# Optimization experiments

Hardware: AMD Instinct MI355X
Metric: run time of the kernel (lower is better)

## Reference

```python
import jax, jax.numpy as jnp
import numpy as np

B, TOK, D, H, L = 64, 20, 512, 8, 4
S = 512          # tokens per half
HD = D // H
ODIM = 32        # encoder_output_dim


def _ln(x, g, b):
    m = x.mean(-1, keepdims=True)
    v = ((x - m) ** 2).mean(-1, keepdims=True)
    return (x - m) / jnp.sqrt(v + 1e-5) * g + b


def _alibi_slopes(h):
    # mirrors FlashAttentionBlock.build_alibi_slopes (base=2.0)
    base = 2.0
    return jnp.asarray([1.0 / base ** (i // (h // base)) for i in range(h)], dtype=jnp.float32)


def setup_inputs() -> dict:
    key = jax.random.key(0)
    ks = jax.random.split(key, 16)
    r = lambda i, shape, s=0.02: jax.random.normal(ks[i], shape, jnp.float32) * s
    return {
        'x': jax.random.normal(ks[0], (B, 2 * S * TOK), jnp.float32),
        'in_W': r(1, (TOK, D)), 'in_b': jnp.zeros((D,)),
        'qkv_W': r(2, (L, D, 3 * D)), 'qkv_b': jnp.zeros((L, 3 * D)),
        'ln1_g': jnp.ones((L, D)), 'ln1_b': jnp.zeros((L, D)),
        'ffn_W1': r(3, (L, D, 4 * D)), 'ffn_b1': jnp.zeros((L, 4 * D)),
        'ffn_W2': r(4, (L, 4 * D, D)), 'ffn_b2': jnp.zeros((L, D)),
        'ln2_g': jnp.ones((L, D)), 'ln2_b': jnp.zeros((L, D)),
        'out_W': r(5, (D, ODIM)), 'out_b': jnp.zeros((ODIM,)),
        'd1_W': r(6, (2 * S * ODIM, 256)), 'd1_b': jnp.zeros((256,)),
        'bn1_g': jnp.ones((256,)), 'bn1_b': jnp.zeros((256,)),
        'bn1_m': jnp.zeros((256,)), 'bn1_v': jnp.ones((256,)),
        'd2_W': r(7, (256, 128)), 'd2_b': jnp.zeros((128,)),
        'bn2_g': jnp.ones((128,)), 'bn2_b': jnp.zeros((128,)),
        'bn2_m': jnp.zeros((128,)), 'bn2_v': jnp.ones((128,)),
        'fin_W': r(8, (128, 1)), 'fin_b': jnp.zeros((1,)),
    }


def _forward(x, in_W, in_b, qkv_W, qkv_b, ln1_g, ln1_b, ffn_W1, ffn_b1,
             ffn_W2, ffn_b2, ln2_g, ln2_b, out_W, out_b,
             d1_W, d1_b, bn1_g, bn1_b, bn1_m, bn1_v,
             d2_W, d2_b, bn2_g, bn2_b, bn2_m, bn2_v, fin_W, fin_b):
    slopes = _alibi_slopes(H)                                   # [H]
    pos = jnp.arange(S)
    # non-causal ALiBi bias: -slope * |i - j|, shape [H, S, S]
    bias = -slopes[:, None, None] * jnp.abs(pos[:, None] - pos[None, :]).astype(jnp.float32)
    scale = 1.0 / np.sqrt(HD).astype(np.float32)

    def encode(xh):
        b = xh.shape[0]
        t = xh.reshape(b, S, TOK) @ in_W + in_b                 # [b, S, D]
        for l in range(L):
            res = t
            qkv = (t @ qkv_W[l] + qkv_b[l]).reshape(b, S, 3, H, HD)
            q, k, v = qkv[:, :, 0], qkv[:, :, 1], qkv[:, :, 2]  # [b, S, H, HD]
            scores = jnp.einsum('bqhd,bkhd->bhqk', q, k) * scale + bias[None]
            attn = jax.nn.softmax(scores, axis=-1)
            o = jnp.einsum('bhqk,bkhd->bqhd', attn, v).reshape(b, S, D)
            t = _ln(res + o, ln1_g[l], ln1_b[l])
            res = t
            f = jax.nn.relu(t @ ffn_W1[l] + ffn_b1[l]) @ ffn_W2[l] + ffn_b2[l]
            t = _ln(res + f, ln2_g[l], ln2_b[l])
        return (t @ out_W + out_b).reshape(b, -1)               # [b, S*ODIM]

    half = S * TOK
    h = jnp.concatenate([encode(x[:, :half]), encode(x[:, half:])], axis=-1)
    bn = lambda z, g, bb, m, v: (z - m) / jnp.sqrt(v + 1e-5) * g + bb
    h = bn(jax.nn.relu(h @ d1_W + d1_b), bn1_g, bn1_b, bn1_m, bn1_v)
    h = bn(jax.nn.relu(h @ d2_W + d2_b), bn2_g, bn2_b, bn2_m, bn2_v)
    return (h @ fin_W + fin_b).squeeze(-1)                      # [B]


def reference(x, in_W, in_b, qkv_W, qkv_b, ln1_g, ln1_b, ffn_W1, ffn_b1,
              ffn_W2, ffn_b2, ln2_g, ln2_b, out_W, out_b,
              d1_W, d1_b, bn1_g, bn1_b, bn1_m, bn1_v,
              d2_W, d2_b, bn2_g, bn2_b, bn2_m, bn2_v, fin_W, fin_b):
    return _forward(x, in_W, in_b, qkv_W, qkv_b, ln1_g, ln1_b, ffn_W1, ffn_b1,
                    ffn_W2, ffn_b2, ln2_g, ln2_b, out_W, out_b,
                    d1_W, d1_b, bn1_g, bn1_b, bn1_m, bn1_v,
                    d2_W, d2_b, bn2_g, bn2_b, bn2_m, bn2_v, fin_W, fin_b)
```

## Files before the change

kernel.cpp:

```cpp
#include <hip/hip_runtime.h>

#define DEV __device__ __forceinline__

using bf16x8 = __attribute__((ext_vector_type(8))) __bf16;
using f32x4  = __attribute__((ext_vector_type(4))) float;
using u16x8  = __attribute__((ext_vector_type(8))) unsigned short;

DEV unsigned short f2bf(float f) {
  unsigned u = __builtin_bit_cast(unsigned, f);
  u += 0x7fffu + ((u >> 16) & 1u);
  return (unsigned short)(u >> 16);
}
DEV float bf2f(unsigned short h) {
  unsigned u = ((unsigned)h) << 16;
  return __builtin_bit_cast(float, u);
}
DEV f32x4 mfma16(u16x8 a, u16x8 b, f32x4 c) {
  return __builtin_amdgcn_mfma_f32_16x16x32_bf16(
      __builtin_bit_cast(bf16x8, a), __builtin_bit_cast(bf16x8, b), c, 0, 0, 0);
}
DEV f32x4 zero4() { f32x4 z = {0.f, 0.f, 0.f, 0.f}; return z; }

DEV void glds16(const unsigned short* g, unsigned short* l) {
  __builtin_amdgcn_global_load_lds(
      (const __attribute__((address_space(1))) unsigned int*)g,
      (__attribute__((address_space(3))) unsigned int*)l, 16, 0, 0);
}

enum { EPI_BIAS = 0, EPI_RELU = 1, EPI_OUT = 2 };

template <int EPI>
__global__ __launch_bounds__(256) void gemm_k(
    const unsigned short* __restrict__ A, const unsigned short* __restrict__ Bt,
    const float* __restrict__ bias, unsigned short* __restrict__ C, int N, int K) {
  __shared__ unsigned short As[128 * 64];
  __shared__ unsigned short Bs[128 * 64];
  const int tid = threadIdx.x;
  const int lane = tid & 63, wv = tid >> 6;
  const int q = lane >> 4, ln = lane & 15;
  const int wr = wv >> 1, wc = wv & 1;

  const int Nt = gridDim.x, Mt = gridDim.y;
  const int lin = blockIdx.x + Nt * blockIdx.y;
  const int xcd = lin & 7;
  const int j = lin >> 3;
  const int mi = xcd * (Mt >> 3) + j / Nt;
  const int ni = j % Nt;
  const int m0 = mi << 7, n0 = ni << 7;

  f32x4 acc[4][4];
#pragma unroll
  for (int i = 0; i < 4; ++i)
#pragma unroll
    for (int jj = 0; jj < 4; ++jj) acc[i][jj] = zero4();

  const int ra = lane >> 3;
  const int ca = ((lane & 7) ^ ra) << 3;
  const unsigned short* Ap = A + (size_t)(m0 + wv * 32 + ra) * K + ca;
  const unsigned short* Bp = Bt + (size_t)(n0 + wv * 32 + ra) * K + ca;
  unsigned short* AsW = As + wv * 2048;
  unsigned short* BsW = Bs + wv * 2048;
  const int ln7 = ln & 7;

  for (int kb = 0; kb < K; kb += 64) {
    __syncthreads();
#pragma unroll
    for (int t = 0; t < 4; ++t) {
      glds16(Ap + (size_t)(t * 8) * K + kb, AsW + t * 512);
      glds16(Bp + (size_t)(t * 8) * K + kb, BsW + t * 512);
    }
    __syncthreads();
#pragma unroll
    for (int kk = 0; kk < 2; ++kk) {
      const int c = kk * 4 + q;
      const int lo = ln * 64 + ((c ^ ln7) << 3);
      u16x8 af[4];
#pragma unroll
      for (int mt = 0; mt < 4; ++mt)
        af[mt] = *(const u16x8*)(As + (wr * 64 + mt * 16) * 64 + lo);
#pragma unroll
      for (int nt = 0; nt < 4; ++nt) {
        u16x8 bf = *(const u16x8*)(Bs + (wc * 64 + nt * 16) * 64 + lo);
#pragma unroll
        for (int mt = 0; mt < 4; ++mt) acc[mt][nt] = mfma16(af[mt], bf, acc[mt][nt]);
      }
    }
  }

#pragma unroll
  for (int mt = 0; mt < 4; ++mt) {
    const int rowb = m0 + wr * 64 + mt * 16 + q * 4;
#pragma unroll
    for (int nt = 0; nt < 4; ++nt) {
      const int col = n0 + wc * 64 + nt * 16 + ln;
      if (EPI == EPI_OUT && col >= 32) continue;
      const float bs = bias[col];
      const int ldc = (EPI == EPI_OUT) ? 32 : N;
#pragma unroll
      for (int r = 0; r < 4; ++r) {
        float v = acc[mt][nt][r] + bs;
        if (EPI == EPI_RELU) v = fmaxf(v, 0.f);
        C[(size_t)(rowb + r) * ldc + col] = f2bf(v);
      }
    }
  }
}

__global__ __launch_bounds__(256) void vt_k(const unsigned short* __restrict__ big,
                                            unsigned short* __restrict__ vt) {
  __shared__ unsigned short td[64 * 72];
  const int tid = threadIdx.x;
  const int sh = blockIdx.x;
  const int seq = sh >> 3, h = sh & 7;
  const int kt = blockIdx.y;
  {
    const int key = tid >> 2, hdc = (tid & 3) << 4;
    const unsigned short* src =
        big + ((size_t)seq * 512 + kt * 64 + key) * 1536 + 1024 + h * 64 + hdc;
    *(u16x8*)(td + key * 72 + hdc) = *(const u16x8*)src;
    *(u16x8*)(td + key * 72 + hdc + 8) = *(const u16x8*)(src + 8);
  }
  __syncthreads();
  {
    const int hd = tid >> 2, kc = (tid & 3) << 4;
    u16x8 a, b;
#pragma unroll
    for (int j = 0; j < 8; ++j) a[j] = td[(kc + j) * 72 + hd];
#pragma unroll
    for (int j = 0; j < 8; ++j) b[j] = td[(kc + 8 + j) * 72 + hd];
    unsigned short* dst = vt + ((size_t)sh * 64 + hd) * 512 + kt * 64 + kc;
    *(u16x8*)dst = a;
    *(u16x8*)(dst + 8) = b;
  }
}

__global__ __launch_bounds__(256) void attn_k(const unsigned short* __restrict__ qkv,
                                              const unsigned short* __restrict__ vt,
                                              unsigned short* __restrict__ o) {
  __shared__ unsigned short Qs[128 * 72];
  __shared__ unsigned short Ks[64 * 72];
  __shared__ unsigned short Vts[64 * 72];
  __shared__ unsigned short Ps[128 * 72];
  const int tid = threadIdx.x;
  const int lane = tid & 63, w = tid >> 6, q = lane >> 4, ln = lane & 15;
  const int bh = blockIdx.x;
  const int seq = bh >> 3, h = bh & 7;
  const int qt = blockIdx.y;
  const size_t tokb = (size_t)seq * 512;
  const int qoff = h * 64, koff = 512 + h * 64;
  const float c1 = 0.125f * 1.44269504f;
  const float c2 = ((h < 4) ? 1.0f : 0.5f) * 1.44269504f;

#pragma unroll
  for (int p = 0; p < 4; ++p) {
    int c = p * 256 + tid;
    int row = c >> 3, cc = (c & 7) << 3;
    u16x8 v = *(const u16x8*)(qkv + (tokb + qt * 128 + row) * 1536 + qoff + cc);
    *(u16x8*)(Qs + row * 72 + cc) = v;
  }
  __syncthreads();
  u16x8 aq[2][2];
#pragma unroll
  for (int mt = 0; mt < 2; ++mt)
#pragma unroll
    for (int kc = 0; kc < 2; ++kc)
      aq[mt][kc] = *(const u16x8*)(Qs + (w * 32 + mt * 16 + ln) * 72 + kc * 32 + q * 8);

  float lacc[2][4];
  f32x4 o_acc[2][4];
#pragma unroll
  for (int mt = 0; mt < 2; ++mt)
#pragma unroll
    for (int r = 0; r < 4; ++r) lacc[mt][r] = 0.f;
#pragma unroll
  for (int mt = 0; mt < 2; ++mt)
#pragma unroll
    for (int ht = 0; ht < 4; ++ht) o_acc[mt][ht] = zero4();

  const int krow = tid >> 3, kcc = (tid & 7) << 3;
  const int vhd = tid >> 2, vc = (tid & 3) << 4;
  const unsigned short* vbase = vt + ((size_t)bh * 64 + vhd) * 512 + vc;

  for (int kt = 0; kt < 8; ++kt) {
    __syncthreads();
    {
      u16x8 v0 = *(const u16x8*)(qkv + (tokb + kt * 64 + krow) * 1536 + koff + kcc);
      u16x8 v1 = *(const u16x8*)(qkv + (tokb + kt * 64 + krow + 32) * 1536 + koff + kcc);
      *(u16x8*)(Ks + krow * 72 + kcc) = v0;
      *(u16x8*)(Ks + (krow + 32) * 72 + kcc) = v1;
      u16x8 w0 = *(const u16x8*)(vbase + kt * 64);
      u16x8 w1 = *(const u16x8*)(vbase + kt * 64 + 8);
      *(u16x8*)(Vts + vhd * 72 + vc) = w0;
      *(u16x8*)(Vts + vhd * 72 + vc + 8) = w1;
    }
    __syncthreads();

    f32x4 sacc[2][4];
#pragma unroll
    for (int mt = 0; mt < 2; ++mt)
#pragma unroll
      for (int nt = 0; nt < 4; ++nt) sacc[mt][nt] = zero4();
#pragma unroll
    for (int nt = 0; nt < 4; ++nt)
#pragma unroll
      for (int kc = 0; kc < 2; ++kc) {
        u16x8 bk = *(const u16x8*)(Ks + (nt * 16 + ln) * 72 + kc * 32 + q * 8);
#pragma unroll
        for (int mt = 0; mt < 2; ++mt) sacc[mt][nt] = mfma16(aq[mt][kc], bk, sacc[mt][nt]);
      }

    const float kbase = (float)(kt * 64 + ln);
#pragma unroll
    for (int mt = 0; mt < 2; ++mt) {
      const float qpb = (float)(qt * 128 + w * 32 + mt * 16 + q * 4);
#pragma unroll
      for (int nt = 0; nt < 4; ++nt) {
        const float kp = kbase + (float)(nt * 16);
#pragma unroll
        for (int r = 0; r < 4; ++r) {
          const float ad = fabsf(qpb + (float)r - kp);
          const float p = exp2f(fmaf(sacc[mt][nt][r], c1, -c2 * ad));
          const unsigned u = __builtin_bit_cast(unsigned, p);
          const unsigned short pb = (unsigned short)((u + 0x8000u) >> 16);
          Ps[(w * 32 + mt * 16 + q * 4 + r) * 72 + nt * 16 + ln] = pb;
          lacc[mt][r] += bf2f(pb);
        }
      }
    }
#pragma unroll
    for (int kc = 0; kc < 2; ++kc) {
      u16x8 pa[2];
#pragma unroll
      for (int mt = 0; mt < 2; ++mt)
        pa[mt] = *(const u16x8*)(Ps + (w * 32 + mt * 16 + ln) * 72 + kc * 32 + q * 8);
#pragma unroll
      for (int ht = 0; ht < 4; ++ht) {
        u16x8 bv = *(const u16x8*)(Vts + (ht * 16 + ln) * 72 + kc * 32 + q * 8);
#pragma unroll
        for (int mt = 0; mt < 2; ++mt) o_acc[mt][ht] = mfma16(pa[mt], bv, o_acc[mt][ht]);
      }
    }
  }

  float rl[2][4];
#pragma unroll
  for (int mt = 0; mt < 2; ++mt)
#pragma unroll
    for (int r = 0; r < 4; ++r) {
      float l = lacc[mt][r];
#pragma unroll
      for (int msk = 1; msk < 16; msk <<= 1) l += __shfl_xor(l, msk, 64);
      rl[mt][r] = 1.0f / l;
    }

#pragma unroll
  for (int mt = 0; mt < 2; ++mt)
#pragma unroll
    for (int ht = 0; ht < 4; ++ht)
#pragma unroll
      for (int r = 0; r < 4; ++r) {
        const int row = qt * 128 + w * 32 + mt * 16 + q * 4 + r;
        const float val = o_acc[mt][ht][r] * rl[mt][r];
        o[(tokb + row) * 512 + h * 64 + ht * 16 + ln] = f2bf(val);
      }
}

__global__ __launch_bounds__(256) void ln_k(const unsigned short* res,
                                            const unsigned short* __restrict__ y,
                                            const float* __restrict__ g,
                                            const float* __restrict__ b,
                                            unsigned short* out) {
  const int lane = threadIdx.x & 63, wv = threadIdx.x >> 6;
  const size_t row = (size_t)blockIdx.x * 4 + wv;
  const size_t base = row * 512 + lane * 8;
  u16x8 rv = *(const u16x8*)(res + base);
  u16x8 yv = *(const u16x8*)(y + base);
  float v[8];
  float s = 0.f, s2 = 0.f;
#pragma unroll
  for (int i = 0; i < 8; ++i) {
    v[i] = bf2f(rv[i]) + bf2f(yv[i]);
    s += v[i];
    s2 += v[i] * v[i];
  }
#pragma unroll
  for (int m = 1; m < 64; m <<= 1) {
    s += __shfl_xor(s, m, 64);
    s2 += __shfl_xor(s2, m, 64);
  }
  const float mean = s * (1.f / 512.f);
  const float var = s2 * (1.f / 512.f) - mean * mean;
  const float rstd = rsqrtf(var + 1e-5f);
  const int c = lane * 8;
  u16x8 ov;
#pragma unroll
  for (int i = 0; i < 8; ++i) ov[i] = f2bf((v[i] - mean) * rstd * g[c + i] + b[c + i]);
  *(u16x8*)(out + base) = ov;
}

__global__ __launch_bounds__(256) void transpose_w(const float* __restrict__ in,
                                                   unsigned short* __restrict__ out,
                                                   int Kin, int Nin, int Kout, int Nout) {
  __shared__ float tile[32][33];
  const int nb = blockIdx.x * 32, kb = blockIdx.y * 32;
  const int tx = threadIdx.x & 31, ty = threadIdx.x >> 5;
#pragma unroll
  for (int i = 0; i < 32; i += 8) {
    int k = kb + ty + i, n = nb + tx;
    tile[ty + i][tx] = (k < Kin && n < Nin) ? in[(size_t)k * Nin + n] : 0.f;
  }
  __syncthreads();
#pragma unroll
  for (int i = 0; i < 32; i += 8) {
    int n = nb + ty + i, k = kb + tx;
    if (n < Nout && k < Kout) out[(size_t)n * Kout + k] = f2bf(tile[tx][ty + i]);
  }
}

__global__ __launch_bounds__(256) void xpad_k(const float* __restrict__ x,
                                              unsigned short* __restrict__ xp) {
  const int idx = blockIdx.x * 256 + threadIdx.x;
  const int tok = idx >> 6, k = idx & 63;
  const int seq = tok >> 9, s = tok & 511;
  const int hf = seq >> 6, b = seq & 63;
  float v = 0.f;
  if (k < 20) v = x[(size_t)b * 20480 + hf * 10240 + s * 20 + k];
  xp[idx] = f2bf(v);
}

__global__ __launch_bounds__(256) void d1_part(const unsigned short* __restrict__ enc,
                                               const float* __restrict__ W,
                                               float* __restrict__ pz) {
  __shared__ float ef[64 * 128];
  const int tid = threadIdx.x;
  const int kb = blockIdx.x * 128;
  const int hf = kb >> 14;
  const int j0 = kb & 16383;
  {
    const int m = tid >> 2, c = (tid & 3) * 32;
    const unsigned short* src = enc + (size_t)hf * 1048576 + (size_t)m * 16384 + j0 + c;
#pragma unroll
    for (int i = 0; i < 4; ++i) {
      u16x8 v = *(const u16x8*)(src + i * 8);
#pragma unroll
      for (int jj = 0; jj < 8; ++jj) ef[m * 128 + c + i * 8 + jj] = bf2f(v[jj]);
    }
  }
  __syncthreads();
  const int n = tid;
  float acc[64];
#pragma unroll
  for (int m = 0; m < 64; ++m) acc[m] = 0.f;
  for (int kc = 0; kc < 128; kc += 4) {
    const float w0 = W[(size_t)(kb + kc) * 256 + n];
    const float w1 = W[(size_t)(kb + kc + 1) * 256 + n];
    const float w2 = W[(size_t)(kb + kc + 2) * 256 + n];
    const float w3 = W[(size_t)(kb + kc + 3) * 256 + n];
#pragma unroll
    for (int m = 0; m < 64; ++m) {
      const f32x4 e = *(const f32x4*)(ef + m * 128 + kc);
      acc[m] += e[0] * w0 + e[1] * w1 + e[2] * w2 + e[3] * w3;
    }
  }
#pragma unroll
  for (int m = 0; m < 64; ++m)
    pz[(size_t)(blockIdx.x * 64 + m) * 256 + n] = acc[m];
}

__global__ __launch_bounds__(256) void d1_fin(const float* __restrict__ pz,
                                              const float* __restrict__ d1b,
                                              const float* __restrict__ g,
                                              const float* __restrict__ b,
                                              const float* __restrict__ mm,
                                              const float* __restrict__ vv,
                                              float* __restrict__ h1) {
  const int m = blockIdx.x, n = threadIdx.x;
  float a = d1b[n];
  for (int sl = 0; sl < 256; ++sl) a += pz[(size_t)(sl * 64 + m) * 256 + n];
  a = fmaxf(a, 0.f);
  a = (a - mm[n]) * rsqrtf(vv[n] + 1e-5f) * g[n] + b[n];
  h1[m * 256 + n] = a;
}

__global__ __launch_bounds__(128) void d2_k(const float* __restrict__ h1,
                                            const float* __restrict__ W,
                                            const float* __restrict__ bb,
                                            const float* __restrict__ g,
                                            const float* __restrict__ b,
                                            const float* __restrict__ mm,
                                            const float* __restrict__ vv,
                                            float* __restrict__ h2) {
  __shared__ float hs[256];
  const int m = blockIdx.x, n = threadIdx.x;
  hs[n] = h1[m * 256 + n];
  hs[n + 128] = h1[m * 256 + n + 128];
  __syncthreads();
  float a = bb[n];
#pragma unroll 8
  for (int k = 0; k < 256; ++k) a += hs[k] * W[k * 128 + n];
  a = fmaxf(a, 0.f);
  a = (a - mm[n]) * rsqrtf(vv[n] + 1e-5f) * g[n] + b[n];
  h2[m * 128 + n] = a;
}

__global__ __launch_bounds__(64) void fin_k(const float* __restrict__ h2,
                                            const float* __restrict__ W,
                                            const float* __restrict__ fb,
                                            float* __restrict__ out) {
  const int m = threadIdx.x;
  float a = fb[0];
#pragma unroll 8
  for (int k = 0; k < 128; ++k) a += h2[m * 128 + k] * W[k];
  out[m] = a;
}

extern "C" void kernel_launch(void* const* d_in, const int* in_sizes, int n_in,
                              void* d_out, int out_size, void* d_ws, size_t ws_size,
                              hipStream_t stream) {
  const float* x      = (const float*)d_in[0];
  const float* in_W   = (const float*)d_in[1];
  const float* in_b   = (const float*)d_in[2];
  const float* qkv_W  = (const float*)d_in[3];
  const float* qkv_b  = (const float*)d_in[4];
  const float* ln1_g  = (const float*)d_in[5];
  const float* ln1_b  = (const float*)d_in[6];
  const float* ffn_W1 = (const float*)d_in[7];
  const float* ffn_b1 = (const float*)d_in[8];
  const float* ffn_W2 = (const float*)d_in[9];
  const float* ffn_b2 = (const float*)d_in[10];
  const float* ln2_g  = (const float*)d_in[11];
  const float* ln2_b  = (const float*)d_in[12];
  const float* out_W  = (const float*)d_in[13];
  const float* out_b  = (const float*)d_in[14];
  const float* d1W    = (const float*)d_in[15];
  const float* d1b    = (const float*)d_in[16];
  const float* bn1g   = (const float*)d_in[17];
  const float* bn1b   = (const float*)d_in[18];
  const float* bn1m   = (const float*)d_in[19];
  const float* bn1v   = (const float*)d_in[20];
  const float* d2W    = (const float*)d_in[21];
  const float* d2b    = (const float*)d_in[22];
  const float* bn2g   = (const float*)d_in[23];
  const float* bn2b   = (const float*)d_in[24];
  const float* bn2m   = (const float*)d_in[25];
  const float* bn2v   = (const float*)d_in[26];
  const float* finW   = (const float*)d_in[27];
  const float* finb   = (const float*)d_in[28];
  (void)in_sizes; (void)n_in; (void)out_size; (void)ws_size;

  char* ws = (char*)d_ws;
  size_t off = 0;
  auto alloc = [&](size_t bytes) {
    char* p = ws + off;
    off += (bytes + 255) & ~(size_t)255;
    return p;
  };
  unsigned short* t     = (unsigned short*)alloc(32768ull * 512 * 2);
  unsigned short* big   = (unsigned short*)alloc(32768ull * 2048 * 2);
  unsigned short* ob    = (unsigned short*)alloc(32768ull * 512 * 2);
  unsigned short* xpad  = (unsigned short*)alloc(65536ull * 64 * 2);
  unsigned short* enc   = (unsigned short*)alloc(65536ull * 32 * 2);
  unsigned short* inWt  = (unsigned short*)alloc(512ull * 64 * 2);
  unsigned short* qkvWt = (unsigned short*)alloc(4ull * 1536 * 512 * 2);
  unsigned short* f1Wt  = (unsigned short*)alloc(4ull * 2048 * 512 * 2);
  unsigned short* f2Wt  = (unsigned short*)alloc(4ull * 512 * 2048 * 2);
  unsigned short* outWt = (unsigned short*)alloc(128ull * 512 * 2);
  float* h1 = (float*)alloc(64ull * 256 * 4);
  float* h2 = (float*)alloc(64ull * 128 * 4);
  float* pz = (float*)big;
  unsigned short* vtb = big + (size_t)32768 * 1536;

  xpad_k<<<16384, 256, 0, stream>>>(x, xpad);
  transpose_w<<<dim3(16, 2), 256, 0, stream>>>(in_W, inWt, 20, 512, 64, 512);
  transpose_w<<<dim3(4, 16), 256, 0, stream>>>(out_W, outWt, 512, 32, 512, 128);
  for (int l = 0; l < 4; ++l) {
    transpose_w<<<dim3(48, 16), 256, 0, stream>>>(qkv_W + (size_t)l * 512 * 1536,
                                                  qkvWt + (size_t)l * 1536 * 512, 512, 1536, 512, 1536);
    transpose_w<<<dim3(64, 16), 256, 0, stream>>>(ffn_W1 + (size_t)l * 512 * 2048,
                                                  f1Wt + (size_t)l * 2048 * 512, 512, 2048, 512, 2048);
    transpose_w<<<dim3(16, 64), 256, 0, stream>>>(ffn_W2 + (size_t)l * 2048 * 512,
                                                  f2Wt + (size_t)l * 512 * 2048, 2048, 512, 2048, 512);
  }

  for (int hf = 0; hf < 2; ++hf) {
    gemm_k<EPI_BIAS><<<dim3(4, 256), 256, 0, stream>>>(xpad + (size_t)hf * 32768 * 64, inWt, in_b, t, 512, 64);
    for (int l = 0; l < 4; ++l) {
      gemm_k<EPI_BIAS><<<dim3(12, 256), 256, 0, stream>>>(t, qkvWt + (size_t)l * 1536 * 512,
                                                          qkv_b + l * 1536, big, 1536, 512);
      vt_k<<<dim3(512, 8), 256, 0, stream>>>(big, vtb);
      attn_k<<<dim3(512, 4), 256, 0, stream>>>(big, vtb, ob);
      ln_k<<<8192, 256, 0, stream>>>(t, ob, ln1_g + l * 512, ln1_b + l * 512, t);
      gemm_k<EPI_RELU><<<dim3(16, 256), 256, 0, stream>>>(t, f1Wt + (size_t)l * 2048 * 512,
                                                          ffn_b1 + l * 2048, big, 2048, 512);
      gemm_k<EPI_BIAS><<<dim3(4, 256), 256, 0, stream>>>(big, f2Wt + (size_t)l * 512 * 2048,
                                                         ffn_b2 + l * 512, ob, 512, 2048);
      ln_k<<<8192, 256, 0, stream>>>(t, ob, ln2_g + l * 512, ln2_b + l * 512, t);
    }
    gemm_k<EPI_OUT><<<dim3(1, 256), 256, 0, stream>>>(t, outWt, out_b,
                                                      enc + (size_t)hf * 32768 * 32, 128, 512);
  }

  d1_part<<<256, 256, 0, stream>>>(enc, d1W, pz);
  d1_fin<<<64, 256, 0, stream>>>(pz, d1b, bn1g, bn1b, bn1m, bn1v, h1);
  d2_k<<<64, 128, 0, stream>>>(h1, d2W, d2b, bn2g, bn2b, bn2m, bn2v, h2);
  fin_k<<<1, 64, 0, stream>>>(h2, finW, finb, (float*)d_out);
}
```

Before: 3.400 ms.

## Add 256x256-tile double-buffered GEMM kernel for encoder projections

```diff
diff --git a/kernel.cpp b/kernel.cpp
--- a/kernel.cpp
+++ b/kernel.cpp
@@ -28,6 +28,118 @@
 }
 
 enum { EPI_BIAS = 0, EPI_RELU = 1, EPI_OUT = 2 };
+
+template <int EPI>
+__global__ __launch_bounds__(512, 2) void gemm256_k(
+    const unsigned short* __restrict__ A, const unsigned short* __restrict__ Bt,
+    const float* __restrict__ bias, unsigned short* __restrict__ C, int N, int K) {
+  __shared__ unsigned short As[2][8192];
+  __shared__ unsigned short Bs[2][8192];
+  const int tid = threadIdx.x;
+  const int lane = tid & 63, wv = tid >> 6;
+  const int q = lane >> 4, ln = lane & 15;
+  const int wr = wv >> 2, wc = wv & 3;
+
+  const int Nt = gridDim.x, Mt = gridDim.y;
+  const int lin = blockIdx.x + Nt * blockIdx.y;
+  const int xcd = lin & 7;
+  const int j = lin >> 3;
+  const int mi = xcd * (Mt >> 3) + j / Nt;
+  const int ni = j % Nt;
+  const int m0 = mi << 8, n0 = ni << 8;
+
+  f32x4 acc[8][4];
+#pragma unroll
+  for (int i = 0; i < 8; ++i)
+#pragma unroll
+    for (int jj = 0; jj < 4; ++jj) acc[i][jj] = zero4();
+
+  const int srow = wv * 16 + (lane >> 2);
+  const int scol = (((lane & 3) ^ ((lane >> 3) & 3)) << 3);
+  const unsigned short* Ap = A + (size_t)(m0 + srow) * K + scol;
+  const unsigned short* Bp = Bt + (size_t)(n0 + srow) * K + scol;
+
+  auto STAGE = [&](int buf, int kb) {
+    unsigned short* ab = &As[buf][wv * 512];
+    unsigned short* bb = &Bs[buf][wv * 512];
+    glds16(Ap + kb, ab);
+    glds16(Ap + (size_t)128 * K + kb, ab + 4096);
+    glds16(Bp + kb, bb);
+    glds16(Bp + (size_t)128 * K + kb, bb + 4096);
+  };
+
+  const int sw = ((q ^ ((ln >> 1) & 3)) << 3);
+  const int NTt = K >> 5;
+
+  STAGE(0, 0);
+  if (NTt > 1) {
+    STAGE(1, 32);
+    asm volatile("s_waitcnt vmcnt(4)" ::: "memory");
+  } else {
+    asm volatile("s_waitcnt vmcnt(0)" ::: "memory");
+  }
+  __builtin_amdgcn_sched_barrier(0);
+  __builtin_amdgcn_s_barrier();
+  __builtin_amdgcn_sched_barrier(0);
+
+  for (int t = 0; t < NTt; ++t) {
+    const int cur = t & 1;
+    u16x8 af[4], bf[4], ag[4];
+#pragma unroll
+    for (int mt = 0; mt < 4; ++mt)
+      af[mt] = *(const u16x8*)(&As[cur][(wr * 128 + mt * 16 + ln) * 32 + sw]);
+#pragma unroll
+    for (int nt = 0; nt < 4; ++nt)
+      bf[nt] = *(const u16x8*)(&Bs[cur][(wc * 64 + nt * 16 + ln) * 32 + sw]);
+    __builtin_amdgcn_s_setprio(1);
+#pragma unroll
+    for (int nt = 0; nt < 4; ++nt)
+#pragma unroll
+      for (int mt = 0; mt < 4; ++mt) acc[mt][nt] = mfma16(af[mt], bf[nt], acc[mt][nt]);
+    __builtin_amdgcn_s_setprio(0);
+#pragma unroll
+    for (int mt = 0; mt < 4; ++mt)
+      ag[mt] = *(const u16x8*)(&As[cur][(wr * 128 + (mt + 4) * 16 + ln) * 32 + sw]);
+    asm volatile("s_waitcnt lgkmcnt(0)" ::: "memory");
+    __builtin_amdgcn_sched_barrier(0);
+    __builtin_amdgcn_s_barrier();
+    __builtin_amdgcn_sched_barrier(0);
+    if (t + 2 < NTt) STAGE(cur, (t + 2) * 32);
+    __builtin_amdgcn_s_setprio(1);
+#pragma unroll
+    for (int nt = 0; nt < 4; ++nt)
+#pragma unroll
+      for (int mt = 0; mt < 4; ++mt)
+        acc[mt + 4][nt] = mfma16(ag[mt], bf[nt], acc[mt + 4][nt]);
+    __builtin_amdgcn_s_setprio(0);
+    if (t < NTt - 1) {
+      if (t + 2 < NTt) {
+        asm volatile("s_waitcnt vmcnt(4)" ::: "memory");
+      } else {
+        asm volatile("s_waitcnt vmcnt(0)" ::: "memory");
+      }
+      __builtin_amdgcn_sched_barrier(0);
+      __builtin_amdgcn_s_barrier();
+      __builtin_amdgcn_sched_barrier(0);
+    }
+  }
+
+#pragma unroll
+  for (int mt = 0; mt < 8; ++mt) {
+    const int rowb = m0 + wr * 128 + mt * 16 + q * 4;
+#pragma unroll
+    for (int nt = 0; nt < 4; ++nt) {
+      const int col = n0 + wc * 64 + nt * 16 + ln;
+      const float bs = bias[col];
+#pragma unroll
+      for (int r = 0; r < 4; ++r) {
+        float v = acc[mt][nt][r] + bs;
+        if (EPI == EPI_RELU) v = fmaxf(v, 0.f);
+        C[(size_t)(rowb + r) * N + col] = f2bf(v);
+      }
+    }
+  }
+}
 
 template <int EPI>
 __global__ __launch_bounds__(256) void gemm_k(
@@ -483,17 +595,17 @@
   }
 
   for (int hf = 0; hf < 2; ++hf) {
-    gemm_k<EPI_BIAS><<<dim3(4, 256), 256, 0, stream>>>(xpad + (size_t)hf * 32768 * 64, inWt, in_b, t, 512, 64);
+    gemm256_k<EPI_BIAS><<<dim3(2, 128), 512, 0, stream>>>(xpad + (size_t)hf * 32768 * 64, inWt, in_b, t, 512, 64);
     for (int l = 0; l < 4; ++l) {
-      gemm_k<EPI_BIAS><<<dim3(12, 256), 256, 0, stream>>>(t, qkvWt + (size_t)l * 1536 * 512,
-                                                          qkv_b + l * 1536, big, 1536, 512);
+      gemm256_k<EPI_BIAS><<<dim3(6, 128), 512, 0, stream>>>(t, qkvWt + (size_t)l * 1536 * 512,
+                                                            qkv_b + l * 1536, big, 1536, 512);
       vt_k<<<dim3(512, 8), 256, 0, stream>>>(big, vtb);
       attn_k<<<dim3(512, 4), 256, 0, stream>>>(big, vtb, ob);
       ln_k<<<8192, 256, 0, stream>>>(t, ob, ln1_g + l * 512, ln1_b + l * 512, t);
-      gemm_k<EPI_RELU><<<dim3(16, 256), 256, 0, stream>>>(t, f1Wt + (size_t)l * 2048 * 512,
-                                                          ffn_b1 + l * 2048, big, 2048, 512);
-      gemm_k<EPI_BIAS><<<dim3(4, 256), 256, 0, stream>>>(big, f2Wt + (size_t)l * 512 * 2048,
-                                                         ffn_b2 + l * 512, ob, 512, 2048);
+      gemm256_k<EPI_RELU><<<dim3(8, 128), 512, 0, stream>>>(t, f1Wt + (size_t)l * 2048 * 512,
+                                                            ffn_b1 + l * 2048, big, 2048, 512);
+      gemm256_k<EPI_BIAS><<<dim3(2, 128), 512, 0, stream>>>(big, f2Wt + (size_t)l * 512 * 2048,
+                                                            ffn_b2 + l * 512, ob, 512, 2048);
       ln_k<<<8192, 256, 0, stream>>>(t, ob, ln2_g + l * 512, ln2_b + l * 512, t);
     }
     gemm_k<EPI_OUT><<<dim3(1, 256), 256, 0, stream>>>(t, outWt, out_b,
```

Result: faster. 3.295 ms (-3.1%).
